# Optimization experiments

Hardware: AMD Instinct MI355X
Metric: run time of the kernel (lower is better)

The kernel has to match this reference:

```python
import jax, jax.numpy as jnp
import numpy as np

B, N, D, H, E, K = 8, 4096, 128, 256, 16, 2


def setup_inputs() -> dict:
    key = jax.random.key(0)
    ks = jax.random.split(key, 11)
    sc = 0.05
    return {
        "x":   jax.random.normal(ks[0], (B, N, D), jnp.float32),
        "Wg":  jax.random.normal(ks[1], (D, E), jnp.float32) * sc,
        "bg":  jnp.zeros((E,), jnp.float32),
        "W1":  jax.random.normal(ks[2], (E, D, H), jnp.float32) * sc,
        "b1":  jnp.zeros((E, H), jnp.float32),
        "W2":  jax.random.normal(ks[3], (E, H, D), jnp.float32) * sc,
        "b2":  jnp.zeros((E, D), jnp.float32),
        "Wu1": jax.random.normal(ks[4], (D, H), jnp.float32) * sc,
        "bu1": jnp.zeros((H,), jnp.float32),
        "Wu2": jax.random.normal(ks[5], (H, D), jnp.float32) * sc,
        "bu2": jnp.zeros((D,), jnp.float32),
    }


def reference(x, Wg, bg, W1, b1, W2, b2, Wu1, bu1, Wu2, bu2):
    b, n, d = x.shape
    xt = x.reshape(b * n, d)                       # [T, D]
    T = xt.shape[0]

    # gating: top-k logits kept, rest -inf, then softmax -> zeros off top-k
    logits = xt @ Wg + bg                          # [T, E]
    topv, topi = jax.lax.top_k(logits, K)          # [T, K]
    mask = jnp.full_like(logits, -jnp.inf)
    mask = mask.at[jnp.arange(T)[:, None], topi].set(topv)
    gate = jax.nn.softmax(mask, axis=-1)           # [T, E]

    # dense all-expert MLP (matches original torch.stack over experts)
    h = jax.nn.relu(jnp.einsum('td,edh->teh', xt, W1) + b1)   # [T, E, H]
    eo = jnp.einsum('teh,ehd->ted', h, W2) + b2               # [T, E, D]

    # universal expert scaled by omega = 1 - max gate
    omega = 1.0 - jnp.max(gate, axis=1, keepdims=True)        # [T, 1]
    uni = omega * (jax.nn.relu(xt @ Wu1 + bu1) @ Wu2 + bu2)   # [T, D]

    out = jnp.einsum('te,ted->td', gate, eo) + uni
    return out.reshape(b, n, d)
```

## Files before the change

kernel.cpp:

```cpp
#include <hip/hip_runtime.h>
#include <hip/hip_bf16.h>

constexpr int kT = 32768;
constexpr int kD = 128;
constexpr int kH = 256;
constexpr int kE = 16;

typedef __bf16 bf16x8 __attribute__((ext_vector_type(8)));
typedef unsigned short u16x8 __attribute__((ext_vector_type(8)));
typedef float f32x4 __attribute__((ext_vector_type(4)));

#define LDX 136
#define LDQ 72

constexpr int NB_TP   = 272;
constexpr int NB_GATE = kT / 64;
constexpr int CNT_STRIDE = 32;
constexpr int MOE_GRID = 1552;

__device__ __forceinline__ unsigned short f2bf(float f) {
  unsigned int u = __float_as_uint(f);
  u += 0x7FFFu + ((u >> 16) & 1u);
  return (unsigned short)(u >> 16);
}
__device__ __forceinline__ float bf2f(unsigned short s) {
  return __uint_as_float((unsigned int)s << 16);
}

__global__ __launch_bounds__(256) void front_kernel(
    const float* __restrict__ x, const float* __restrict__ Wg,
    const float* __restrict__ bg,
    const float* __restrict__ W1, const float* __restrict__ W2,
    const float* __restrict__ Wu1, const float* __restrict__ Wu2,
    unsigned short* __restrict__ xb, unsigned short* __restrict__ W1t,
    unsigned short* __restrict__ W2t, unsigned short* __restrict__ Wu1t,
    unsigned short* __restrict__ Wu2t,
    int* __restrict__ cnt, int* __restrict__ btok, float* __restrict__ bgate,
    int* __restrict__ tpos)
{
  __shared__ __align__(16) char smem[46848];
  const int tid = threadIdx.x;
  const int b = blockIdx.x;

  if (b < NB_TP) {
    int bb = b;
    const float* src; unsigned short* dst; int R, C, r0, c0;
    if (bb < 136) {
      int m = bb >> 3, t8 = bb & 7;
      R = 128; C = 256;
      src = (m < 16) ? W1 + (size_t)m * 32768 : Wu1;
      dst = (m < 16) ? W1t + (size_t)m * 32768 : Wu1t;
      r0 = (t8 & 1) * 64; c0 = (t8 >> 1) * 64;
    } else {
      bb -= 136;
      int m = bb >> 3, t8 = bb & 7;
      R = 256; C = 128;
      src = (m < 16) ? W2 + (size_t)m * 32768 : Wu2;
      dst = (m < 16) ? W2t + (size_t)m * 32768 : Wu2t;
      r0 = (t8 >> 1) * 64; c0 = (t8 & 1) * 64;
    }
    unsigned short (*tl)[72] = reinterpret_cast<unsigned short(*)[72]>(smem);
#pragma unroll
    for (int i = 0; i < 4; ++i) {
      int s = i * 256 + tid;
      int r = s >> 4, c4 = s & 15;
      float4 v = *reinterpret_cast<const float4*>(&src[(size_t)(r0 + r) * C + c0 + c4 * 4]);
      tl[c4 * 4 + 0][r] = f2bf(v.x);
      tl[c4 * 4 + 1][r] = f2bf(v.y);
      tl[c4 * 4 + 2][r] = f2bf(v.z);
      tl[c4 * 4 + 3][r] = f2bf(v.w);
    }
    __syncthreads();
#pragma unroll
    for (int i = 0; i < 2; ++i) {
      int s = i * 256 + tid;
      int c = s >> 3, seg = s & 7;
      uint4 v = *reinterpret_cast<const uint4*>(&tl[c][seg * 8]);
      *reinterpret_cast<uint4*>(&dst[(size_t)(c0 + c) * R + r0 + seg * 8]) = v;
    }
    return;
  }

  {
    float* sWt = reinterpret_cast<float*>(smem);
    float* sX  = reinterpret_cast<float*>(smem + 8448);
    float* sL  = reinterpret_cast<float*>(smem + 42240);
    int* hcnt  = reinterpret_cast<int*>(smem + 46592);
    int* hbase = reinterpret_cast<int*>(smem + 46656);
    int* hb16  = reinterpret_cast<int*>(smem + 46720);
    const int t0 = (b - NB_TP) * 64;

    if (tid < kE) hcnt[tid] = 0;
    for (int i = tid; i < kD * kE; i += 256) {
      int d = i >> 4, e = i & 15;
      sWt[e * 132 + d] = Wg[i];
    }
    const float4* xv = reinterpret_cast<const float4*>(x + (size_t)t0 * kD);
    for (int i = tid; i < 64 * kD / 4; i += 256) {
      int r = i >> 5, c4 = i & 31;
      *reinterpret_cast<float4*>(&sX[r * 132 + c4 * 4]) = xv[i];
    }
    __syncthreads();

    const int e = tid & 15, tq = tid >> 4;
    const double bgd = (double)bg[e];
    const float4* wr = reinterpret_cast<const float4*>(&sWt[e * 132]);
    double acc[4] = {0.0, 0.0, 0.0, 0.0};
#pragma unroll
    for (int d4 = 0; d4 < 32; ++d4) {
      float4 wa = wr[d4];
#pragma unroll
      for (int p = 0; p < 4; ++p) {
        float4 xa = *reinterpret_cast<const float4*>(&sX[(p * 16 + tq) * 132 + d4 * 4]);
        acc[p] += (double)xa.x * (double)wa.x + (double)xa.y * (double)wa.y
                + (double)xa.z * (double)wa.z + (double)xa.w * (double)wa.w;
      }
    }
#pragma unroll
    for (int p = 0; p < 4; ++p)
      sL[(p * 16 + tq) * 17 + e] = (float)(acc[p] + bgd);
#pragma unroll
    for (int p = 0; p < 4; ++p) {
      int idx = p * 256 + tid;
      int r = idx >> 4, c8 = (idx & 15) * 8;
      const float* sp = &sX[r * 132 + c8];
      u16x8 v;
#pragma unroll
      for (int j = 0; j < 8; ++j) v[j] = f2bf(sp[j]);
      *reinterpret_cast<u16x8*>(&xb[(size_t)(t0 + r) * kD + c8]) = v;
    }
    __syncthreads();

    int e0 = 0, e1 = 0, lp0 = 0, lp1 = 0;
    float g0 = 0.f, g1 = 0.f;
    const int t = t0 + tid;
    if (tid < 64) {
      float v0 = -3.4e38f, v1 = -3.4e38f;
      for (int i = 0; i < kE; ++i) {
        float v = sL[tid * 17 + i];
        if (v > v0) { v1 = v0; e1 = e0; v0 = v; e0 = i; }
        else if (v > v1) { v1 = v; e1 = i; }
      }
      float r = expf(v1 - v0);
      g0 = 1.f / (1.f + r);
      g1 = 1.f - g0;
      lp0 = atomicAdd(&hcnt[e0], 1);
      lp1 = atomicAdd(&hcnt[e1], 1);
    }
    if (tid == 0) hb16[0] = atomicAdd(&cnt[16 * CNT_STRIDE], 64);
    __syncthreads();
    if (tid < kE)
      hbase[tid] = atomicAdd(&cnt[tid * CNT_STRIDE], hcnt[tid]);
    __syncthreads();
    if (tid < 64) {
      int p0 = hbase[e0] + lp0;
      btok[e0 * kT + p0] = t; bgate[e0 * kT + p0] = g0;
      int p1 = hbase[e1] + lp1;
      btok[e1 * kT + p1] = t; bgate[e1 * kT + p1] = g1;
      int p2 = hb16[0] + tid;
      btok[16 * kT + p2] = t; bgate[16 * kT + p2] = 1.f - g0;
      tpos[2 * t]     = (e0 << 16) | p0;
      tpos[2 * t + 1] = (e1 << 16) | p1;
    }
  }
}

__global__ __launch_bounds__(256) void moe_kernel(
    const unsigned short* __restrict__ xb,
    const unsigned short* __restrict__ W1t,
    const unsigned short* __restrict__ W2t,
    const unsigned short* __restrict__ Wu1t,
    const unsigned short* __restrict__ Wu2t,
    const float* __restrict__ b1, const float* __restrict__ b2,
    const float* __restrict__ bu1, const float* __restrict__ bu2,
    const int* __restrict__ cnt, const int* __restrict__ btok,
    const float* __restrict__ bgate,
    unsigned short* __restrict__ eo, float* __restrict__ out)
{
  __shared__ alignas(16) char smem[27136];
  unsigned short* xs = reinterpret_cast<unsigned short*>(smem);
  unsigned short* hs = reinterpret_cast<unsigned short*>(smem + 17408);
  int*   toks = reinterpret_cast<int*>(smem + 26624);
  float* gts  = reinterpret_cast<float*>(smem + 26880);
  unsigned short* stB = reinterpret_cast<unsigned short*>(smem);
  float* stF = reinterpret_cast<float*>(smem);
  const int tid = threadIdx.x;
  const int bid = blockIdx.x;

  int c17[17];
#pragma unroll
  for (int i = 0; i < 17; ++i) c17[i] = cnt[i * CNT_STRIDE];
  int e = -1, tile = 0, eobase = 0, accb = 0;
#pragma unroll
  for (int i = 0; i < 17; ++i) {
    int tl = (c17[i] + 63) >> 6;
    if (e < 0) {
      if (bid < accb + tl) { e = i; tile = bid - accb; }
      else { accb += tl; if (i < 16) eobase += c17[i]; }
    }
  }
  if (e < 0) return;
  const int rows = min(64, c17[e] - tile * 64);

  const int w = tid >> 6, l = tid & 63, lr = l & 15, lg = l >> 4;
  const int gr = tid >> 4, gc = (tid & 15) * 8;
  const f32x4 z4 = {0.f, 0.f, 0.f, 0.f};

  const unsigned short* Bw1 = (e < 16) ? W1t + (size_t)e * kH * kD : Wu1t;
  const unsigned short* Bw2 = (e < 16) ? W2t + (size_t)e * kD * kH : Wu2t;
  const float* bs1 = (e < 16) ? b1 + (size_t)e * kH : bu1;
  const float* bs2 = (e < 16) ? b2 + (size_t)e * kD : bu2;

  {
    int tokR[4]; float gtR[4];
#pragma unroll
    for (int p = 0; p < 4; ++p) {
      int r = p * 16 + gr; bool v = r < rows; int bi2 = e * kT + tile * 64 + r;
      tokR[p] = v ? btok[bi2] : 0;
      gtR[p]  = v ? bgate[bi2] : 0.f;
    }
#pragma unroll
    for (int p = 0; p < 4; ++p) {
      uint4 v = *reinterpret_cast<const uint4*>(xb + (size_t)tokR[p] * kD + gc);
      *reinterpret_cast<uint4*>(&xs[(p * 16 + gr) * LDX + gc]) = v;
    }
    if ((tid & 15) == 0) {
#pragma unroll
      for (int p = 0; p < 4; ++p) {
        toks[p * 16 + gr] = tokR[p];
        gts[p * 16 + gr]  = gtR[p];
      }
    }
  }
  float b2v[2];
#pragma unroll
  for (int n = 0; n < 2; ++n) b2v[n] = bs2[w * 32 + n * 16 + lr];
  f32x4 acc2[4][2];
#pragma unroll
  for (int m = 0; m < 4; ++m)
#pragma unroll
    for (int n = 0; n < 2; ++n) acc2[m][n] = z4;
  __syncthreads();

#pragma unroll
  for (int hq = 0; hq < 4; ++hq) {
    const int hcol = hq * 64 + w * 16 + lr;
    bf16x8 Bf[4];
#pragma unroll
    for (int kk = 0; kk < 4; ++kk)
      Bf[kk] = *reinterpret_cast<const bf16x8*>(
          Bw1 + (size_t)hcol * kD + kk * 32 + lg * 8);
    const float b1q = bs1[hcol];
    f32x4 acc[4];
#pragma unroll
    for (int m = 0; m < 4; ++m) acc[m] = z4;
#pragma unroll
    for (int kk = 0; kk < 4; ++kk) {
      bf16x8 a[4];
#pragma unroll
      for (int m = 0; m < 4; ++m)
        a[m] = *reinterpret_cast<const bf16x8*>(xs + (m * 16 + lr) * LDX + kk * 32 + lg * 8);
#pragma unroll
      for (int m = 0; m < 4; ++m)
        acc[m] = __builtin_amdgcn_mfma_f32_16x16x32_bf16(a[m], Bf[kk], acc[m], 0, 0, 0);
    }
#pragma unroll
    for (int m = 0; m < 4; ++m)
#pragma unroll
      for (int q = 0; q < 4; ++q) {
        float v = acc[m][q] + b1q;
        v = fmaxf(v, 0.f);
        hs[(m * 16 + lg * 4 + q) * LDQ + w * 16 + lr] = f2bf(v);
      }
    __syncthreads();

    bf16x8 B2f[2][2];
#pragma unroll
    for (int n = 0; n < 2; ++n)
#pragma unroll
      for (int k2 = 0; k2 < 2; ++k2)
        B2f[n][k2] = *reinterpret_cast<const bf16x8*>(
            Bw2 + (size_t)(w * 32 + n * 16 + lr) * kH + hq * 64 + k2 * 32 + lg * 8);
#pragma unroll
    for (int k2 = 0; k2 < 2; ++k2) {
      bf16x8 a[4];
#pragma unroll
      for (int m = 0; m < 4; ++m)
        a[m] = *reinterpret_cast<const bf16x8*>(hs + (m * 16 + lr) * LDQ + k2 * 32 + lg * 8);
#pragma unroll
      for (int m = 0; m < 4; ++m)
#pragma unroll
        for (int n = 0; n < 2; ++n)
          acc2[m][n] = __builtin_amdgcn_mfma_f32_16x16x32_bf16(a[m], B2f[n][k2], acc2[m][n], 0, 0, 0);
    }
    __syncthreads();
  }

  if (e < 16) {
#pragma unroll
    for (int m = 0; m < 4; ++m)
#pragma unroll
      for (int q = 0; q < 4; ++q) {
        int r = m * 16 + lg * 4 + q;
        float g = gts[r];
#pragma unroll
        for (int n = 0; n < 2; ++n)
          stB[r * LDX + w * 32 + n * 16 + lr] = f2bf(g * (acc2[m][n][q] + b2v[n]));
      }
    __syncthreads();
    unsigned short* dst = eo + (size_t)(eobase + tile * 64) * kD;
#pragma unroll
    for (int j = 0; j < 4; ++j) {
      int gidx = j * 256 + tid;
      int r = gidx >> 4, seg = gidx & 15;
      if (r < rows) {
        uint4 v = *reinterpret_cast<const uint4*>(&stB[r * LDX + seg * 8]);
        *reinterpret_cast<uint4*>(dst + (size_t)r * kD + seg * 8) = v;
      }
    }
  } else {
#pragma unroll
    for (int ch = 0; ch < 2; ++ch) {
      if ((w >> 1) == ch) {
#pragma unroll
        for (int m = 0; m < 4; ++m)
#pragma unroll
          for (int q = 0; q < 4; ++q) {
            int r = m * 16 + lg * 4 + q;
            float g = gts[r];
#pragma unroll
            for (int n = 0; n < 2; ++n)
              stF[r * 68 + (w & 1) * 32 + n * 16 + lr] = g * (acc2[m][n][q] + b2v[n]);
          }
      }
      __syncthreads();
#pragma unroll
      for (int j = 0; j < 4; ++j) {
        int gidx = j * 256 + tid;
        int r = gidx >> 4, seg = gidx & 15;
        if (r < rows) {
          int tok = toks[r];
          float4 v = *reinterpret_cast<const float4*>(&stF[r * 68 + seg * 4]);
          *reinterpret_cast<float4*>(out + (size_t)tok * kD + ch * 64 + seg * 4) = v;
        }
      }
      __syncthreads();
    }
  }
}

__global__ __launch_bounds__(256) void combine_kernel(
    const int* __restrict__ cnt, const int* __restrict__ tpos,
    const unsigned short* __restrict__ eo, float* __restrict__ out)
{
  __shared__ int base[16];
  const int tid = threadIdx.x;
  if (tid < 16) {
    int s = 0;
    for (int i = 0; i < tid; ++i) s += cnt[i * CNT_STRIDE];
    base[tid] = s;
  }
  __syncthreads();
  const int tk = blockIdx.x * 16 + (tid >> 4);
  const int c = tid & 15;
  int a0 = tpos[2 * tk], a1 = tpos[2 * tk + 1];
  size_t r0 = (size_t)(base[a0 >> 16] + (a0 & 0xffff)) * kD + c * 8;
  size_t r1 = (size_t)(base[a1 >> 16] + (a1 & 0xffff)) * kD + c * 8;
  u16x8 v0 = *reinterpret_cast<const u16x8*>(eo + r0);
  u16x8 v1 = *reinterpret_cast<const u16x8*>(eo + r1);
  float s[8];
#pragma unroll
  for (int j = 0; j < 8; ++j) s[j] = bf2f(v0[j]) + bf2f(v1[j]);
  float4* op = reinterpret_cast<float4*>(out + (size_t)tk * kD + c * 8);
  float4 o0 = op[0], o1 = op[1];
  o0.x += s[0]; o0.y += s[1]; o0.z += s[2]; o0.w += s[3];
  o1.x += s[4]; o1.y += s[5]; o1.z += s[6]; o1.w += s[7];
  op[0] = o0; op[1] = o1;
}

extern "C" void kernel_launch(void* const* d_in, const int* in_sizes, int n_in,
                              void* d_out, int out_size, void* d_ws, size_t ws_size,
                              hipStream_t stream) {
  (void)in_sizes; (void)n_in; (void)out_size; (void)ws_size;
  const float* x   = (const float*)d_in[0];
  const float* Wg  = (const float*)d_in[1];
  const float* bg  = (const float*)d_in[2];
  const float* W1  = (const float*)d_in[3];
  const float* b1  = (const float*)d_in[4];
  const float* W2  = (const float*)d_in[5];
  const float* b2  = (const float*)d_in[6];
  const float* Wu1 = (const float*)d_in[7];
  const float* bu1 = (const float*)d_in[8];
  const float* Wu2 = (const float*)d_in[9];
  const float* bu2 = (const float*)d_in[10];
  float* out = (float*)d_out;

  char* ws = (char*)d_ws;
  constexpr size_t OFF_XB    = 0;
  constexpr size_t OFF_W1T   = 8388608;
  constexpr size_t OFF_W2T   = 9437184;
  constexpr size_t OFF_WU1T  = 10485760;
  constexpr size_t OFF_WU2T  = 10551296;
  constexpr size_t OFF_CNT   = 10616832;
  constexpr size_t OFF_TPOS  = 10620928;
  constexpr size_t OFF_BTOK  = 10883072;
  constexpr size_t OFF_BGATE = 13111296;
  constexpr size_t OFF_EO    = 15339520;

  unsigned short* xb   = (unsigned short*)(ws + OFF_XB);
  unsigned short* W1t  = (unsigned short*)(ws + OFF_W1T);
  unsigned short* W2t  = (unsigned short*)(ws + OFF_W2T);
  unsigned short* Wu1t = (unsigned short*)(ws + OFF_WU1T);
  unsigned short* Wu2t = (unsigned short*)(ws + OFF_WU2T);
  int*   cnt   = (int*)(ws + OFF_CNT);
  int*   tpos  = (int*)(ws + OFF_TPOS);
  int*   btok  = (int*)(ws + OFF_BTOK);
  float* bgate = (float*)(ws + OFF_BGATE);
  unsigned short* eo = (unsigned short*)(ws + OFF_EO);

  hipMemsetAsync(cnt, 0, 17 * CNT_STRIDE * sizeof(int), stream);
  front_kernel<<<NB_TP + NB_GATE, 256, 0, stream>>>(
      x, Wg, bg, W1, W2, Wu1, Wu2,
      xb, W1t, W2t, Wu1t, Wu2t, cnt, btok, bgate, tpos);
  moe_kernel<<<MOE_GRID, 256, 0, stream>>>(
      xb, W1t, W2t, Wu1t, Wu2t, b1, b2, bu1, bu2, cnt, btok, bgate, eo, out);
  combine_kernel<<<kT / 16, 256, 0, stream>>>(cnt, tpos, eo, out);
}
```

Measured before the change: 81.90 us.

## Double-buffer expert weight fragments in registers and use LDS-only barriers

```diff
diff --git a/kernel.cpp b/kernel.cpp
--- a/kernel.cpp
+++ b/kernel.cpp
@@ -25,6 +25,11 @@
 }
 __device__ __forceinline__ float bf2f(unsigned short s) {
   return __uint_as_float((unsigned int)s << 16);
+}
+__device__ __forceinline__ void bar_lgkm() {
+  asm volatile("s_waitcnt lgkmcnt(0)" ::: "memory");
+  __builtin_amdgcn_s_barrier();
+  asm volatile("" ::: "memory");
 }
 
 __global__ __launch_bounds__(256) void front_kernel(
@@ -164,6 +169,20 @@
     }
   }
 }
+
+#define LOAD_W1(BUF, HQ)                                                      \
+  _Pragma("unroll")                                                           \
+  for (int kk = 0; kk < 4; ++kk)                                              \
+    W1r[BUF][kk] = *reinterpret_cast<const bf16x8*>(                          \
+        Bw1 + (size_t)((HQ) * 64 + w * 16 + lr) * kD + kk * 32 + lg * 8);
+
+#define LOAD_W2(BUF, HQ)                                                      \
+  _Pragma("unroll")                                                           \
+  for (int n = 0; n < 2; ++n)                                                 \
+    _Pragma("unroll")                                                         \
+    for (int k2 = 0; k2 < 2; ++k2)                                            \
+      W2r[BUF][n * 2 + k2] = *reinterpret_cast<const bf16x8*>(                \
+          Bw2 + (size_t)(w * 32 + n * 16 + lr) * kH + (HQ) * 64 + k2 * 32 + lg * 8);
 
 __global__ __launch_bounds__(256) void moe_kernel(
     const unsigned short* __restrict__ xb,
@@ -211,6 +230,15 @@
   const float* bs1 = (e < 16) ? b1 + (size_t)e * kH : bu1;
   const float* bs2 = (e < 16) ? b2 + (size_t)e * kD : bu2;
 
+  bf16x8 W1r[2][4], W2r[2][4];
+  LOAD_W1(0, 0); LOAD_W2(0, 0);
+  float b1q[4];
+#pragma unroll
+  for (int hq = 0; hq < 4; ++hq) b1q[hq] = bs1[hq * 64 + w * 16 + lr];
+  float b2v[2];
+#pragma unroll
+  for (int n = 0; n < 2; ++n) b2v[n] = bs2[w * 32 + n * 16 + lr];
+
   {
     int tokR[4]; float gtR[4];
 #pragma unroll
@@ -232,25 +260,21 @@
       }
     }
   }
-  float b2v[2];
-#pragma unroll
-  for (int n = 0; n < 2; ++n) b2v[n] = bs2[w * 32 + n * 16 + lr];
   f32x4 acc2[4][2];
 #pragma unroll
   for (int m = 0; m < 4; ++m)
 #pragma unroll
     for (int n = 0; n < 2; ++n) acc2[m][n] = z4;
-  __syncthreads();
+  bar_lgkm();
 
 #pragma unroll
   for (int hq = 0; hq < 4; ++hq) {
-    const int hcol = hq * 64 + w * 16 + lr;
-    bf16x8 Bf[4];
-#pragma unroll
-    for (int kk = 0; kk < 4; ++kk)
-      Bf[kk] = *reinterpret_cast<const bf16x8*>(
-          Bw1 + (size_t)hcol * kD + kk * 32 + lg * 8);
-    const float b1q = bs1[hcol];
+    const int cur = hq & 1;
+    if (hq < 3) {
+      const int nxt = cur ^ 1;
+      LOAD_W1(nxt, hq + 1);
+      LOAD_W2(nxt, hq + 1);
+    }
     f32x4 acc[4];
 #pragma unroll
     for (int m = 0; m < 4; ++m) acc[m] = z4;
@@ -262,25 +286,17 @@
         a[m] = *reinterpret_cast<const bf16x8*>(xs + (m * 16 + lr) * LDX + kk * 32 + lg * 8);
 #pragma unroll
       for (int m = 0; m < 4; ++m)
-        acc[m] = __builtin_amdgcn_mfma_f32_16x16x32_bf16(a[m], Bf[kk], acc[m], 0, 0, 0);
+        acc[m] = __builtin_amdgcn_mfma_f32_16x16x32_bf16(a[m], W1r[cur][kk], acc[m], 0, 0, 0);
     }
 #pragma unroll
     for (int m = 0; m < 4; ++m)
 #pragma unroll
       for (int q = 0; q < 4; ++q) {
-        float v = acc[m][q] + b1q;
+        float v = acc[m][q] + b1q[hq];
         v = fmaxf(v, 0.f);
         hs[(m * 16 + lg * 4 + q) * LDQ + w * 16 + lr] = f2bf(v);
       }
-    __syncthreads();
-
-    bf16x8 B2f[2][2];
-#pragma unroll
-    for (int n = 0; n < 2; ++n)
-#pragma unroll
-      for (int k2 = 0; k2 < 2; ++k2)
-        B2f[n][k2] = *reinterpret_cast<const bf16x8*>(
-            Bw2 + (size_t)(w * 32 + n * 16 + lr) * kH + hq * 64 + k2 * 32 + lg * 8);
+    bar_lgkm();
 #pragma unroll
     for (int k2 = 0; k2 < 2; ++k2) {
       bf16x8 a[4];
@@ -291,9 +307,9 @@
       for (int m = 0; m < 4; ++m)
 #pragma unroll
         for (int n = 0; n < 2; ++n)
-          acc2[m][n] = __builtin_amdgcn_mfma_f32_16x16x32_bf16(a[m], B2f[n][k2], acc2[m][n], 0, 0, 0);
-    }
-    __syncthreads();
+          acc2[m][n] = __builtin_amdgcn_mfma_f32_16x16x32_bf16(a[m], W2r[cur][n * 2 + k2], acc2[m][n], 0, 0, 0);
+    }
+    bar_lgkm();
   }
 
   if (e < 16) {
@@ -307,7 +323,7 @@
         for (int n = 0; n < 2; ++n)
           stB[r * LDX + w * 32 + n * 16 + lr] = f2bf(g * (acc2[m][n][q] + b2v[n]));
       }
-    __syncthreads();
+    bar_lgkm();
     unsigned short* dst = eo + (size_t)(eobase + tile * 64) * kD;
 #pragma unroll
     for (int j = 0; j < 4; ++j) {
@@ -333,7 +349,7 @@
               stF[r * 68 + (w & 1) * 32 + n * 16 + lr] = g * (acc2[m][n][q] + b2v[n]);
           }
       }
-      __syncthreads();
+      bar_lgkm();
 #pragma unroll
       for (int j = 0; j < 4; ++j) {
         int gidx = j * 256 + tid;
@@ -344,7 +360,7 @@
           *reinterpret_cast<float4*>(out + (size_t)tok * kD + ch * 64 + seg * 4) = v;
         }
       }
-      __syncthreads();
+      bar_lgkm();
     }
   }
 }
```

New measurement: 76.06 us (median of 2 runs). 1.08x faster.

## Make MoE kernel persistent with register-resident expert weights and prefetched token tiles

Applied to the files above, without the earlier changes.

```diff
diff --git a/kernel.cpp b/kernel.cpp
--- a/kernel.cpp
+++ b/kernel.cpp
@@ -16,7 +16,7 @@
 constexpr int NB_TP   = 272;
 constexpr int NB_GATE = kT / 64;
 constexpr int CNT_STRIDE = 32;
-constexpr int MOE_GRID = 1552;
+constexpr int MOE_GRID = 512;
 
 __device__ __forceinline__ unsigned short f2bf(float f) {
   unsigned int u = __float_as_uint(f);
@@ -25,6 +25,11 @@
 }
 __device__ __forceinline__ float bf2f(unsigned short s) {
   return __uint_as_float((unsigned int)s << 16);
+}
+__device__ __forceinline__ void bar_lgkm() {
+  asm volatile("s_waitcnt lgkmcnt(0)" ::: "memory");
+  __builtin_amdgcn_s_barrier();
+  asm volatile("" ::: "memory");
 }
 
 __global__ __launch_bounds__(256) void front_kernel(
@@ -165,7 +170,7 @@
   }
 }
 
-__global__ __launch_bounds__(256) void moe_kernel(
+__global__ __launch_bounds__(256, 2) void moe_kernel(
     const unsigned short* __restrict__ xb,
     const unsigned short* __restrict__ W1t,
     const unsigned short* __restrict__ W2t,
@@ -184,24 +189,47 @@
   float* gts  = reinterpret_cast<float*>(smem + 26880);
   unsigned short* stB = reinterpret_cast<unsigned short*>(smem);
   float* stF = reinterpret_cast<float*>(smem);
+  __shared__ int stl[17];
+  __shared__ int sdesc[5];
   const int tid = threadIdx.x;
-  const int bid = blockIdx.x;
-
-  int c17[17];
-#pragma unroll
-  for (int i = 0; i < 17; ++i) c17[i] = cnt[i * CNT_STRIDE];
-  int e = -1, tile = 0, eobase = 0, accb = 0;
-#pragma unroll
-  for (int i = 0; i < 17; ++i) {
-    int tl = (c17[i] + 63) >> 6;
-    if (e < 0) {
-      if (bid < accb + tl) { e = i; tile = bid - accb; }
-      else { accb += tl; if (i < 16) eobase += c17[i]; }
-    }
-  }
-  if (e < 0) return;
-  const int rows = min(64, c17[e] - tile * 64);
-
+
+  if (tid < 17) stl[tid] = cnt[tid * CNT_STRIDE];
+  __syncthreads();
+  if (tid == 0) {
+    int tiles[17], tot = 0;
+    for (int i = 0; i < 17; ++i) { tiles[i] = (stl[i] + 63) >> 6; tot += tiles[i]; }
+    const int G = MOE_GRID;
+    int Be[17], rem[17], sum = 0;
+    for (int i = 0; i < 17; ++i) {
+      int num = G * tiles[i];
+      Be[i] = num / tot;
+      rem[i] = num - Be[i] * tot;
+      sum += Be[i];
+    }
+    int R = G - sum;
+    for (int k = 0; k < R; ++k) {
+      int bi = 0, br = -1;
+      for (int i = 0; i < 17; ++i)
+        if (rem[i] > br) { br = rem[i]; bi = i; }
+      Be[bi] += 1; rem[bi] = -1;
+    }
+    int bb = blockIdx.x, acc = 0, e = -1, Bi = 0, BeE = 1;
+    for (int i = 0; i < 17; ++i) {
+      if (bb < acc + Be[i]) { e = i; Bi = bb - acc; BeE = Be[i]; break; }
+      acc += Be[i];
+    }
+    sdesc[0] = e; sdesc[1] = Bi;
+    sdesc[2] = (e >= 0) ? ((stl[e] + 63) >> 6) : 0;
+    sdesc[3] = BeE;
+    int eb = 0;
+    if (e >= 0 && e < 16) for (int i = 0; i < e; ++i) eb += stl[i];
+    sdesc[4] = eb;
+  }
+  __syncthreads();
+  const int e = sdesc[0], Bi = sdesc[1], tiles_e = sdesc[2], Be = sdesc[3];
+  const int eobase = sdesc[4];
+  if (e < 0 || Bi >= tiles_e) return;
+  const int gcnt = stl[e];
   const int w = tid >> 6, l = tid & 63, lr = l & 15, lg = l >> 4;
   const int gr = tid >> 4, gc = (tid & 15) * 8;
   const f32x4 z4 = {0.f, 0.f, 0.f, 0.f};
@@ -211,19 +239,46 @@
   const float* bs1 = (e < 16) ? b1 + (size_t)e * kH : bu1;
   const float* bs2 = (e < 16) ? b2 + (size_t)e * kD : bu2;
 
-  {
-    int tokR[4]; float gtR[4];
-#pragma unroll
-    for (int p = 0; p < 4; ++p) {
-      int r = p * 16 + gr; bool v = r < rows; int bi2 = e * kT + tile * 64 + r;
-      tokR[p] = v ? btok[bi2] : 0;
-      gtR[p]  = v ? bgate[bi2] : 0.f;
-    }
-#pragma unroll
-    for (int p = 0; p < 4; ++p) {
-      uint4 v = *reinterpret_cast<const uint4*>(xb + (size_t)tokR[p] * kD + gc);
-      *reinterpret_cast<uint4*>(&xs[(p * 16 + gr) * LDX + gc]) = v;
-    }
+  bf16x8 W1r[4][4];
+  bf16x8 W2r[4][4];
+#pragma unroll
+  for (int hq = 0; hq < 4; ++hq)
+#pragma unroll
+    for (int kk = 0; kk < 4; ++kk)
+      W1r[hq][kk] = *reinterpret_cast<const bf16x8*>(
+          Bw1 + (size_t)(hq * 64 + w * 16 + lr) * kD + kk * 32 + lg * 8);
+#pragma unroll
+  for (int hq = 0; hq < 4; ++hq)
+#pragma unroll
+    for (int n = 0; n < 2; ++n)
+#pragma unroll
+      for (int k2 = 0; k2 < 2; ++k2)
+        W2r[hq][n * 2 + k2] = *reinterpret_cast<const bf16x8*>(
+            Bw2 + (size_t)(w * 32 + n * 16 + lr) * kH + hq * 64 + k2 * 32 + lg * 8);
+  float b1q[4], b2v[2];
+#pragma unroll
+  for (int hq = 0; hq < 4; ++hq) b1q[hq] = bs1[hq * 64 + w * 16 + lr];
+#pragma unroll
+  for (int n = 0; n < 2; ++n) b2v[n] = bs2[w * 32 + n * 16 + lr];
+
+  int t = Bi;
+  int rows = min(64, gcnt - t * 64);
+  int tokR[4]; float gtR[4]; uint4 R[4];
+#pragma unroll
+  for (int p = 0; p < 4; ++p) {
+    int r = p * 16 + gr; bool v = r < rows; int bi2 = e * kT + t * 64 + r;
+    tokR[p] = v ? btok[bi2] : 0;
+    gtR[p]  = v ? bgate[bi2] : 0.f;
+  }
+#pragma unroll
+  for (int p = 0; p < 4; ++p)
+    R[p] = *reinterpret_cast<const uint4*>(xb + (size_t)tokR[p] * kD + gc);
+
+  for (;;) {
+    bar_lgkm();
+#pragma unroll
+    for (int p = 0; p < 4; ++p)
+      *reinterpret_cast<uint4*>(&xs[(p * 16 + gr) * LDX + gc]) = R[p];
     if ((tid & 15) == 0) {
 #pragma unroll
       for (int p = 0; p < 4; ++p) {
@@ -231,121 +286,120 @@
         gts[p * 16 + gr]  = gtR[p];
       }
     }
-  }
-  float b2v[2];
-#pragma unroll
-  for (int n = 0; n < 2; ++n) b2v[n] = bs2[w * 32 + n * 16 + lr];
-  f32x4 acc2[4][2];
-#pragma unroll
-  for (int m = 0; m < 4; ++m)
-#pragma unroll
-    for (int n = 0; n < 2; ++n) acc2[m][n] = z4;
-  __syncthreads();
-
-#pragma unroll
-  for (int hq = 0; hq < 4; ++hq) {
-    const int hcol = hq * 64 + w * 16 + lr;
-    bf16x8 Bf[4];
-#pragma unroll
-    for (int kk = 0; kk < 4; ++kk)
-      Bf[kk] = *reinterpret_cast<const bf16x8*>(
-          Bw1 + (size_t)hcol * kD + kk * 32 + lg * 8);
-    const float b1q = bs1[hcol];
-    f32x4 acc[4];
-#pragma unroll
-    for (int m = 0; m < 4; ++m) acc[m] = z4;
-#pragma unroll
-    for (int kk = 0; kk < 4; ++kk) {
-      bf16x8 a[4];
+    int tn = t + Be;
+    bool hasN = tn < tiles_e;
+    int rowsN = 0;
+    if (hasN) {
+      rowsN = min(64, gcnt - tn * 64);
+#pragma unroll
+      for (int p = 0; p < 4; ++p) {
+        int r = p * 16 + gr; bool v = r < rowsN; int bi2 = e * kT + tn * 64 + r;
+        tokR[p] = v ? btok[bi2] : 0;
+        gtR[p]  = v ? bgate[bi2] : 0.f;
+      }
+#pragma unroll
+      for (int p = 0; p < 4; ++p)
+        R[p] = *reinterpret_cast<const uint4*>(xb + (size_t)tokR[p] * kD + gc);
+    }
+    f32x4 acc2[4][2];
+#pragma unroll
+    for (int m = 0; m < 4; ++m)
+#pragma unroll
+      for (int n = 0; n < 2; ++n) acc2[m][n] = z4;
+    bar_lgkm();
+
+#pragma unroll
+    for (int hq = 0; hq < 4; ++hq) {
+      f32x4 acc[4];
+#pragma unroll
+      for (int m = 0; m < 4; ++m) acc[m] = z4;
+#pragma unroll
+      for (int kk = 0; kk < 4; ++kk) {
+        bf16x8 a[4];
+#pragma unroll
+        for (int m = 0; m < 4; ++m)
+          a[m] = *reinterpret_cast<const bf16x8*>(xs + (m * 16 + lr) * LDX + kk * 32 + lg * 8);
+#pragma unroll
+        for (int m = 0; m < 4; ++m)
+          acc[m] = __builtin_amdgcn_mfma_f32_16x16x32_bf16(a[m], W1r[hq][kk], acc[m], 0, 0, 0);
+      }
 #pragma unroll
       for (int m = 0; m < 4; ++m)
-        a[m] = *reinterpret_cast<const bf16x8*>(xs + (m * 16 + lr) * LDX + kk * 32 + lg * 8);
+#pragma unroll
+        for (int q = 0; q < 4; ++q) {
+          float v = acc[m][q] + b1q[hq];
+          v = fmaxf(v, 0.f);
+          hs[(m * 16 + lg * 4 + q) * LDQ + w * 16 + lr] = f2bf(v);
+        }
+      bar_lgkm();
+#pragma unroll
+      for (int k2 = 0; k2 < 2; ++k2) {
+        bf16x8 a[4];
+#pragma unroll
+        for (int m = 0; m < 4; ++m)
+          a[m] = *reinterpret_cast<const bf16x8*>(hs + (m * 16 + lr) * LDQ + k2 * 32 + lg * 8);
+#pragma unroll
+        for (int m = 0; m < 4; ++m)
+#pragma unroll
+          for (int n = 0; n < 2; ++n)
+            acc2[m][n] = __builtin_amdgcn_mfma_f32_16x16x32_bf16(a[m], W2r[hq][n * 2 + k2], acc2[m][n], 0, 0, 0);
+      }
+      bar_lgkm();
+    }
+
+    if (e < 16) {
 #pragma unroll
       for (int m = 0; m < 4; ++m)
-        acc[m] = __builtin_amdgcn_mfma_f32_16x16x32_bf16(a[m], Bf[kk], acc[m], 0, 0, 0);
-    }
-#pragma unroll
-    for (int m = 0; m < 4; ++m)
-#pragma unroll
-      for (int q = 0; q < 4; ++q) {
-        float v = acc[m][q] + b1q;
-        v = fmaxf(v, 0.f);
-        hs[(m * 16 + lg * 4 + q) * LDQ + w * 16 + lr] = f2bf(v);
-      }
-    __syncthreads();
-
-    bf16x8 B2f[2][2];
-#pragma unroll
-    for (int n = 0; n < 2; ++n)
-#pragma unroll
-      for (int k2 = 0; k2 < 2; ++k2)
-        B2f[n][k2] = *reinterpret_cast<const bf16x8*>(
-            Bw2 + (size_t)(w * 32 + n * 16 + lr) * kH + hq * 64 + k2 * 32 + lg * 8);
-#pragma unroll
-    for (int k2 = 0; k2 < 2; ++k2) {
-      bf16x8 a[4];
-#pragma unroll
-      for (int m = 0; m < 4; ++m)
-        a[m] = *reinterpret_cast<const bf16x8*>(hs + (m * 16 + lr) * LDQ + k2 * 32 + lg * 8);
-#pragma unroll
-      for (int m = 0; m < 4; ++m)
-#pragma unroll
-        for (int n = 0; n < 2; ++n)
-          acc2[m][n] = __builtin_amdgcn_mfma_f32_16x16x32_bf16(a[m], B2f[n][k2], acc2[m][n], 0, 0, 0);
-    }
-    __syncthreads();
-  }
-
-  if (e < 16) {
-#pragma unroll
-    for (int m = 0; m < 4; ++m)
-#pragma unroll
-      for (int q = 0; q < 4; ++q) {
-        int r = m * 16 + lg * 4 + q;
-        float g = gts[r];
-#pragma unroll
-        for (int n = 0; n < 2; ++n)
-          stB[r * LDX + w * 32 + n * 16 + lr] = f2bf(g * (acc2[m][n][q] + b2v[n]));
-      }
-    __syncthreads();
-    unsigned short* dst = eo + (size_t)(eobase + tile * 64) * kD;
-#pragma unroll
-    for (int j = 0; j < 4; ++j) {
-      int gidx = j * 256 + tid;
-      int r = gidx >> 4, seg = gidx & 15;
-      if (r < rows) {
-        uint4 v = *reinterpret_cast<const uint4*>(&stB[r * LDX + seg * 8]);
-        *reinterpret_cast<uint4*>(dst + (size_t)r * kD + seg * 8) = v;
-      }
-    }
-  } else {
-#pragma unroll
-    for (int ch = 0; ch < 2; ++ch) {
-      if ((w >> 1) == ch) {
-#pragma unroll
-        for (int m = 0; m < 4; ++m)
-#pragma unroll
-          for (int q = 0; q < 4; ++q) {
-            int r = m * 16 + lg * 4 + q;
-            float g = gts[r];
-#pragma unroll
-            for (int n = 0; n < 2; ++n)
-              stF[r * 68 + (w & 1) * 32 + n * 16 + lr] = g * (acc2[m][n][q] + b2v[n]);
-          }
-      }
-      __syncthreads();
+#pragma unroll
+        for (int q = 0; q < 4; ++q) {
+          int r = m * 16 + lg * 4 + q;
+          float g = gts[r];
+#pragma unroll
+          for (int n = 0; n < 2; ++n)
+            stB[r * LDX + w * 32 + n * 16 + lr] = f2bf(g * (acc2[m][n][q] + b2v[n]));
+        }
+      bar_lgkm();
+      unsigned short* dst = eo + (size_t)(eobase + t * 64) * kD;
 #pragma unroll
       for (int j = 0; j < 4; ++j) {
         int gidx = j * 256 + tid;
         int r = gidx >> 4, seg = gidx & 15;
         if (r < rows) {
-          int tok = toks[r];
-          float4 v = *reinterpret_cast<const float4*>(&stF[r * 68 + seg * 4]);
-          *reinterpret_cast<float4*>(out + (size_t)tok * kD + ch * 64 + seg * 4) = v;
+          uint4 v = *reinterpret_cast<const uint4*>(&stB[r * LDX + seg * 8]);
+          *reinterpret_cast<uint4*>(dst + (size_t)r * kD + seg * 8) = v;
         }
       }
-      __syncthreads();
-    }
+    } else {
+#pragma unroll
+      for (int ch = 0; ch < 2; ++ch) {
+        if ((w >> 1) == ch) {
+#pragma unroll
+          for (int m = 0; m < 4; ++m)
+#pragma unroll
+            for (int q = 0; q < 4; ++q) {
+              int r = m * 16 + lg * 4 + q;
+              float g = gts[r];
+#pragma unroll
+              for (int n = 0; n < 2; ++n)
+                stF[r * 68 + (w & 1) * 32 + n * 16 + lr] = g * (acc2[m][n][q] + b2v[n]);
+            }
+        }
+        bar_lgkm();
+#pragma unroll
+        for (int j = 0; j < 4; ++j) {
+          int gidx = j * 256 + tid;
+          int r = gidx >> 4, seg = gidx & 15;
+          if (r < rows) {
+            int tok = toks[r];
+            float4 v = *reinterpret_cast<const float4*>(&stF[r * 68 + seg * 4]);
+            *reinterpret_cast<float4*>(out + (size_t)tok * kD + ch * 64 + seg * 4) = v;
+          }
+        }
+        bar_lgkm();
+      }
+    }
+    if (!hasN) break;
+    t = tn; rows = rowsN;
   }
 }
 
```

Result: slower. 85.22 us (+4.1%).
